# Kernel optimization log

Hardware: AMD Instinct MI355X
Metric: run time of the kernel (lower is better)

Reference implementation:

```python
import jax, jax.numpy as jnp
import numpy as np

B, P, E, H = 16, 1024, 1024, 16
DH = E // H  # 64


def setup_inputs() -> dict:
    key = jax.random.key(0)
    ks = jax.random.split(key, 7)
    # kaiming_uniform on [H, DH, DH]: bound = sqrt(6 / fan_in), fan_in = DH
    bound = float(np.sqrt(6.0 / DH))
    w_att_val = jax.random.uniform(ks[0], (H, DH, DH), jnp.float32, -bound, bound)
    attention_bias = jax.random.normal(ks[1], (H, P, P), jnp.float32)
    lb = float(1.0 / np.sqrt(E))
    wv_w = jax.random.uniform(ks[2], (E, E), jnp.float32, -lb, lb)
    wv_b = jax.random.uniform(ks[3], (E,), jnp.float32, -lb, lb)
    out_w = jax.random.uniform(ks[4], (E, E), jnp.float32, -lb, lb)
    out_b = jax.random.uniform(ks[5], (E,), jnp.float32, -lb, lb)
    x = jax.random.normal(ks[6], (B, P, E), jnp.float32)
    return {"x": x, "w_att_val": w_att_val, "attention_bias": attention_bias,
            "wv_w": wv_w, "wv_b": wv_b, "out_w": out_w, "out_b": out_b}


def reference(x, w_att_val, attention_bias, wv_w, wv_b, out_w, out_b):
    b, p, e = x.shape
    dh = e // H
    # split heads: [B, H, P, DH]
    x_h = x.reshape(b, p, H, dh).transpose(0, 2, 1, 3)
    # bilinear scores: (x_h @ W) @ x_h^T -> [B, H, P, P]
    xw = jnp.einsum('bhpd,hde->bhpe', x_h, w_att_val)
    scores = jnp.einsum('bhpe,bhqe->bhpq', xw, x_h)
    scores = scores / jnp.sqrt(jnp.asarray(dh, x.dtype)) + attention_bias
    attn = jax.nn.softmax(scores, axis=-1)
    # values: Linear(E, E) then split heads
    vx = x @ wv_w.T + wv_b
    vx = vx.reshape(b, p, H, dh).transpose(0, 2, 1, 3)
    out = jnp.einsum('bhpq,bhqd->bhpd', attn, vx)
    out = out.transpose(0, 2, 1, 3).reshape(b, p, e)
    return out @ out_w.T + out_b
```

## Files before the change

### kernel.cpp

```cpp
#include <hip/hip_runtime.h>

#define PB 16
#define PP 1024
#define PE 1024
#define PH 16
#define PDH 64

typedef __attribute__((ext_vector_type(8))) short bf16x8;
typedef __attribute__((ext_vector_type(4))) short bf16x4;
typedef __attribute__((ext_vector_type(4))) float f32x4;

#define LOG2E 1.44269504088896340736f

__device__ __forceinline__ short f2bf(float f) {
    union { float f; unsigned u; } a;
    a.f = f;
    unsigned u = a.u;
    u += 0x7fffu + ((u >> 16) & 1u);
    return (short)(u >> 16);
}
__device__ __forceinline__ float bf2f(short s) {
    union { unsigned u; float f; } a;
    a.u = ((unsigned)(unsigned short)s) << 16;
    return a.f;
}
__device__ __forceinline__ unsigned cvtpk(float lo, float hi) {
    unsigned r;
    asm("v_cvt_pk_bf16_f32 %0, %1, %2" : "=v"(r) : "v"(lo), "v"(hi));
    return r;
}
union U8 { unsigned u[4]; bf16x8 v; };
__device__ __forceinline__ void async16(const void* g, void* l) {
    __builtin_amdgcn_global_load_lds(
        (const __attribute__((address_space(1))) unsigned int*)g,
        (__attribute__((address_space(3))) unsigned int*)l, 16, 0, 0);
}

__global__ __launch_bounds__(256) void bias_conv(const float* __restrict__ bias,
                                                 short* __restrict__ biasb) {
    size_t idx = ((size_t)blockIdx.x * 256 + threadIdx.x) * 8;
    float4 a = *(const float4*)(bias + idx);
    float4 b = *(const float4*)(bias + idx + 4);
    bf16x8 t = {f2bf(a.x * LOG2E), f2bf(a.y * LOG2E), f2bf(a.z * LOG2E), f2bf(a.w * LOG2E),
                f2bf(b.x * LOG2E), f2bf(b.y * LOG2E), f2bf(b.z * LOG2E), f2bf(b.w * LOG2E)};
    *(bf16x8*)(biasb + idx) = t;
}

__global__ __launch_bounds__(256) void wconv(const float* __restrict__ wvw,
                                             const float* __restrict__ outw,
                                             short* __restrict__ wvwb,
                                             short* __restrict__ outwb) {
    int bid = blockIdx.x;
    const float* src = (bid < 512) ? wvw : outw;
    short* dst = (bid < 512) ? wvwb : outwb;
    int lb = (bid < 512) ? bid : bid - 512;
    size_t idx = ((size_t)lb * 256 + threadIdx.x) * 8;
    float4 a = *(const float4*)(src + idx);
    float4 b = *(const float4*)(src + idx + 4);
    bf16x8 t = {f2bf(a.x), f2bf(a.y), f2bf(a.z), f2bf(a.w),
                f2bf(b.x), f2bf(b.y), f2bf(b.z), f2bf(b.w)};
    *(bf16x8*)(dst + idx) = t;
}

__global__ __launch_bounds__(256) void xw_kernel(const float* __restrict__ x,
                                                 const float* __restrict__ watt,
                                                 short* __restrict__ xw,
                                                 short* __restrict__ xbf) {
    int bid = blockIdx.x;
    int q4 = bid & 3;
    int bh = bid >> 2;
    int h = bh & 15;
    __shared__ short Wt[64][88];

    int tid = threadIdx.x;
    {
        const float* W = watt + (size_t)h * 4096;
        int idx = tid * 16;
        int d = idx >> 6, e0 = idx & 63;
#pragma unroll
        for (int i = 0; i < 16; i += 4) {
            float4 v = *(const float4*)(W + d * 64 + e0 + i);
            Wt[e0 + i + 0][d] = f2bf(v.x);
            Wt[e0 + i + 1][d] = f2bf(v.y);
            Wt[e0 + i + 2][d] = f2bf(v.z);
            Wt[e0 + i + 3][d] = f2bf(v.w);
        }
    }
    __syncthreads();

    int wave = tid >> 6, lane = tid & 63;
    int lm = lane & 15, lq = lane >> 4;

    bf16x8 bfr[4][2];
#pragma unroll
    for (int nt = 0; nt < 4; nt++)
#pragma unroll
        for (int kf = 0; kf < 2; kf++)
            bfr[nt][kf] = *(const bf16x8*)&Wt[nt * 16 + lm][kf * 32 + lq * 8];

    int b = bh >> 4;
    const float QSCALE = 0.125f * LOG2E;
    for (int pass = 0; pass < 4; pass++) {
        int p0 = q4 * 256 + pass * 64 + wave * 16;
        const float* xrow = x + ((size_t)(b * 1024 + p0 + lm)) * 1024 + h * 64;
        short* xorow = xbf + ((size_t)(b * 1024 + p0 + lm)) * 1024 + h * 64;
        bf16x8 af[2];
#pragma unroll
        for (int kf = 0; kf < 2; kf++) {
            float4 v0 = *(const float4*)(xrow + kf * 32 + lq * 8);
            float4 v1 = *(const float4*)(xrow + kf * 32 + lq * 8 + 4);
            bf16x8 t;
            t[0] = f2bf(v0.x); t[1] = f2bf(v0.y); t[2] = f2bf(v0.z); t[3] = f2bf(v0.w);
            t[4] = f2bf(v1.x); t[5] = f2bf(v1.y); t[6] = f2bf(v1.z); t[7] = f2bf(v1.w);
            af[kf] = t;
            *(bf16x8*)(xorow + kf * 32 + lq * 8) = t;
        }
#pragma unroll
        for (int nt = 0; nt < 4; nt++) {
            f32x4 acc = {0.f, 0.f, 0.f, 0.f};
            acc = __builtin_amdgcn_mfma_f32_16x16x32_bf16(af[0], bfr[nt][0], acc, 0, 0, 0);
            acc = __builtin_amdgcn_mfma_f32_16x16x32_bf16(af[1], bfr[nt][1], acc, 0, 0, 0);
            size_t base = ((size_t)bh * 1024 + p0 + lq * 4) * 64 + nt * 16 + lm;
#pragma unroll
            for (int r = 0; r < 4; r++)
                xw[base + (size_t)r * 64] = f2bf(acc[r] * QSCALE);
        }
    }
}

__global__ __launch_bounds__(256) void vx_gemm(const short* __restrict__ xbf,
                                               const short* __restrict__ wvwb,
                                               const float* __restrict__ wvb,
                                               short* __restrict__ vt) {
    int mblk = blockIdx.x >> 3, nblk = blockIdx.x & 7;
    int m0 = mblk * 128, n0 = nblk * 128;
    __shared__ short As[128 * 32];
    __shared__ short Bs[128 * 32];

    int tid = threadIdx.x;
    int wv = tid >> 6, ln = tid & 63;
    int c0 = wv * 2;
    int rrow = ln >> 2, rseg = (ln & 3) * 8;
    const short* gA = xbf + (size_t)(m0 + c0 * 16 + rrow) * 1024 + rseg;
    const short* gB = wvwb + (size_t)(n0 + c0 * 16 + rrow) * 1024 + rseg;
    short* lA = As + c0 * 512;
    short* lB = Bs + c0 * 512;

    int lane = ln, lm = lane & 15, lq = lane >> 4;
    int wm = (wv >> 1) * 64, wn = (wv & 1) * 64;

    f32x4 acc[4][4];
#pragma unroll
    for (int i = 0; i < 4; i++)
#pragma unroll
        for (int j = 0; j < 4; j++) acc[i][j] = (f32x4){0.f, 0.f, 0.f, 0.f};

    for (int k0 = 0; k0 < 1024; k0 += 32) {
        __syncthreads();
        async16(gA + k0, lA);
        async16(gA + k0 + 16 * 1024, lA + 512);
        async16(gB + k0, lB);
        async16(gB + k0 + 16 * 1024, lB + 512);
        __syncthreads();
        bf16x8 af[4], bfr[4];
#pragma unroll
        for (int mt = 0; mt < 4; mt++) af[mt] = *(const bf16x8*)&As[(wm + mt * 16 + lm) * 32 + lq * 8];
#pragma unroll
        for (int nt = 0; nt < 4; nt++) bfr[nt] = *(const bf16x8*)&Bs[(wn + nt * 16 + lm) * 32 + lq * 8];
#pragma unroll
        for (int mt = 0; mt < 4; mt++)
#pragma unroll
            for (int nt = 0; nt < 4; nt++)
                acc[mt][nt] = __builtin_amdgcn_mfma_f32_16x16x32_bf16(af[mt], bfr[nt], acc[mt][nt], 0, 0, 0);
    }

#pragma unroll
    for (int nt = 0; nt < 4; nt++) {
        int e = n0 + wn + nt * 16 + lm;
        float bias = wvb[e];
        int hh = e >> 6, dd = e & 63;
#pragma unroll
        for (int mt = 0; mt < 4; mt++) {
            int pg = m0 + wm + mt * 16 + lq * 4;
            int bb = pg >> 10, pp = pg & 1023;
            bf16x4 pk;
#pragma unroll
            for (int r = 0; r < 4; r++) pk[r] = f2bf(acc[mt][nt][r] + bias);
            *(bf16x4*)(vt + ((size_t)((bb * 16 + hh) * 64 + dd)) * 1024 + pp) = pk;
        }
    }
}

__global__ __launch_bounds__(256, 3) void flash_kernel(const short* __restrict__ xbf,
                                                       const short* __restrict__ xw,
                                                       const short* __restrict__ vt,
                                                       const short* __restrict__ biasb,
                                                       short* __restrict__ obuf) {
    int bid = blockIdx.x;
    int qblk = bid & 7, b = (bid >> 3) & 15, h = bid >> 7;
    int bh = b * 16 + h;
    int q0 = qblk * 128;

    __shared__ short Ks[64][72];
    __shared__ short Vs[64][72];
    __shared__ float Rs[4][36];

    int tid = threadIdx.x, wave = tid >> 6, lane = tid & 63;
    int lm = lane & 15, lq = lane >> 4;

    bf16x8 qa[2][2];
#pragma unroll
    for (int qt = 0; qt < 2; qt++)
#pragma unroll
        for (int kf = 0; kf < 2; kf++)
            qa[qt][kf] = *(const bf16x8*)(xw + ((size_t)bh * 1024 + q0 + wave * 32 + qt * 16 + lm) * 64 + kf * 32 + lq * 8);

    f32x4 o[2][4];
#pragma unroll
    for (int qt = 0; qt < 2; qt++)
#pragma unroll
        for (int dt = 0; dt < 4; dt++) o[qt][dt] = (f32x4){0.f, 0.f, 0.f, 0.f};
    float rs[2] = {0.f, 0.f};

    int ci0 = tid * 2, ci1 = tid * 2 + 1;
    int r0 = ci0 >> 3, s0 = (ci0 & 7) * 8;
    int r1 = ci1 >> 3, s1 = (ci1 & 7) * 8;
    const short* kg = xbf + ((size_t)(b * 1024)) * 1024 + h * 64;
    const short* vg = vt + ((size_t)bh * 64) * 1024;
    const short* bg = biasb + ((size_t)h << 20) + (size_t)(q0 + wave * 32) * 1024;

    bf16x8 kr[2], vr[2];
    bf16x4 br[4][2];
    kr[0] = *(const bf16x8*)(kg + (size_t)r0 * 1024 + s0);
    kr[1] = *(const bf16x8*)(kg + (size_t)r1 * 1024 + s1);
    vr[0] = *(const bf16x8*)(vg + (size_t)r0 * 1024 + s0);
    vr[1] = *(const bf16x8*)(vg + (size_t)r1 * 1024 + s1);
#pragma unroll
    for (int kt = 0; kt < 4; kt++)
#pragma unroll
        for (int qt = 0; qt < 2; qt++)
            br[kt][qt] = *(const bf16x4*)(bg + (size_t)(qt * 16 + lm) * 1024 + kt * 16 + lq * 4);
    *(bf16x8*)&Ks[r0][s0] = kr[0];
    *(bf16x8*)&Ks[r1][s1] = kr[1];
    *(bf16x8*)&Vs[r0][s0] = vr[0];
    *(bf16x8*)&Vs[r1][s1] = vr[1];

    for (int tile = 0; tile < 16; tile++) {
        int kv0 = tile * 64;
        __syncthreads();

        f32x4 s[4][2];
#pragma unroll
        for (int kt = 0; kt < 4; kt++)
#pragma unroll
            for (int qt = 0; qt < 2; qt++) {
                bf16x4 bv = br[kt][qt];
                s[kt][qt] = (f32x4){bf2f(bv[0]), bf2f(bv[1]), bf2f(bv[2]), bf2f(bv[3])};
            }

        if (tile < 15) {
            int kvn = kv0 + 64;
            kr[0] = *(const bf16x8*)(kg + (size_t)(kvn + r0) * 1024 + s0);
            kr[1] = *(const bf16x8*)(kg + (size_t)(kvn + r1) * 1024 + s1);
            vr[0] = *(const bf16x8*)(vg + (size_t)r0 * 1024 + kvn + s0);
            vr[1] = *(const bf16x8*)(vg + (size_t)r1 * 1024 + kvn + s1);
#pragma unroll
            for (int kt = 0; kt < 4; kt++)
#pragma unroll
                for (int qt = 0; qt < 2; qt++)
                    br[kt][qt] = *(const bf16x4*)(bg + (size_t)(qt * 16 + lm) * 1024 + kvn + kt * 16 + lq * 4);
        }

#pragma unroll
        for (int kf = 0; kf < 2; kf++) {
            bf16x8 ka[4];
#pragma unroll
            for (int kt = 0; kt < 4; kt++)
                ka[kt] = *(const bf16x8*)&Ks[kt * 16 + lm][kf * 32 + lq * 8];
#pragma unroll
            for (int kt = 0; kt < 4; kt++)
#pragma unroll
                for (int qt = 0; qt < 2; qt++)
                    s[kt][qt] = __builtin_amdgcn_mfma_f32_16x16x32_bf16(ka[kt], qa[qt][kf], s[kt][qt], 0, 0, 0);
        }

#pragma unroll
        for (int kt = 0; kt < 4; kt++)
#pragma unroll
            for (int qt = 0; qt < 2; qt++)
#pragma unroll
                for (int r = 0; r < 4; r++) {
                    float pv = __builtin_amdgcn_exp2f(s[kt][qt][r]);
                    s[kt][qt][r] = pv;
                    rs[qt] += pv;
                }

#pragma unroll
        for (int kf = 0; kf < 2; kf++) {
            bf16x8 pa[2];
#pragma unroll
            for (int qt = 0; qt < 2; qt++) {
                U8 u;
                u.u[0] = cvtpk(s[kf * 2][qt][0], s[kf * 2][qt][1]);
                u.u[1] = cvtpk(s[kf * 2][qt][2], s[kf * 2][qt][3]);
                u.u[2] = cvtpk(s[kf * 2 + 1][qt][0], s[kf * 2 + 1][qt][1]);
                u.u[3] = cvtpk(s[kf * 2 + 1][qt][2], s[kf * 2 + 1][qt][3]);
                pa[qt] = u.v;
            }
#pragma unroll
            for (int dt = 0; dt < 4; dt++) {
                U8 uv;
                *(bf16x4*)&uv.u[0] = *(const bf16x4*)&Vs[dt * 16 + lm][kf * 32 + lq * 4];
                *(bf16x4*)&uv.u[2] = *(const bf16x4*)&Vs[dt * 16 + lm][kf * 32 + 16 + lq * 4];
#pragma unroll
                for (int qt = 0; qt < 2; qt++)
                    o[qt][dt] = __builtin_amdgcn_mfma_f32_16x16x32_bf16(pa[qt], uv.v, o[qt][dt], 0, 0, 0);
            }
        }

        __syncthreads();
        if (tile < 15) {
            *(bf16x8*)&Ks[r0][s0] = kr[0];
            *(bf16x8*)&Ks[r1][s1] = kr[1];
            *(bf16x8*)&Vs[r0][s0] = vr[0];
            *(bf16x8*)&Vs[r1][s1] = vr[1];
        }
    }

#pragma unroll
    for (int qt = 0; qt < 2; qt++) {
        rs[qt] += __shfl_xor(rs[qt], 16);
        rs[qt] += __shfl_xor(rs[qt], 32);
    }
    if (lq == 0) { Rs[wave][lm] = rs[0]; Rs[wave][16 + lm] = rs[1]; }
    __syncthreads();

#pragma unroll
    for (int qt = 0; qt < 2; qt++) {
        float inv[4];
#pragma unroll
        for (int r = 0; r < 4; r++)
            inv[r] = 1.f / Rs[wave][qt * 16 + lq * 4 + r];
#pragma unroll
        for (int dt = 0; dt < 4; dt++) {
            int e = h * 64 + dt * 16 + lm;
#pragma unroll
            for (int r = 0; r < 4; r++) {
                int p = q0 + wave * 32 + qt * 16 + lq * 4 + r;
                obuf[((size_t)(b * 1024 + p)) * 1024 + e] = f2bf(o[qt][dt][r] * inv[r]);
            }
        }
    }
}

__global__ __launch_bounds__(256) void out_gemm(const short* __restrict__ obuf,
                                                const short* __restrict__ outwb,
                                                const float* __restrict__ outb,
                                                float* __restrict__ out) {
    int mblk = blockIdx.x >> 3, nblk = blockIdx.x & 7;
    int m0 = mblk * 128, n0 = nblk * 128;
    __shared__ short As[128 * 32];
    __shared__ short Bs[128 * 32];

    int tid = threadIdx.x;
    int wv = tid >> 6, ln = tid & 63;
    int c0 = wv * 2;
    int rrow = ln >> 2, rseg = (ln & 3) * 8;
    const short* gA = obuf + (size_t)(m0 + c0 * 16 + rrow) * 1024 + rseg;
    const short* gB = outwb + (size_t)(n0 + c0 * 16 + rrow) * 1024 + rseg;
    short* lA = As + c0 * 512;
    short* lB = Bs + c0 * 512;

    int lm = ln & 15, lq = ln >> 4;
    int wm = (wv >> 1) * 64, wn = (wv & 1) * 64;

    f32x4 acc[4][4];
#pragma unroll
    for (int i = 0; i < 4; i++)
#pragma unroll
        for (int j = 0; j < 4; j++) acc[i][j] = (f32x4){0.f, 0.f, 0.f, 0.f};

    for (int k0 = 0; k0 < 1024; k0 += 32) {
        __syncthreads();
        async16(gA + k0, lA);
        async16(gA + k0 + 16 * 1024, lA + 512);
        async16(gB + k0, lB);
        async16(gB + k0 + 16 * 1024, lB + 512);
        __syncthreads();
        bf16x8 af[4], bfr[4];
#pragma unroll
        for (int mt = 0; mt < 4; mt++) af[mt] = *(const bf16x8*)&As[(wm + mt * 16 + lm) * 32 + lq * 8];
#pragma unroll
        for (int nt = 0; nt < 4; nt++) bfr[nt] = *(const bf16x8*)&Bs[(wn + nt * 16 + lm) * 32 + lq * 8];
#pragma unroll
        for (int mt = 0; mt < 4; mt++)
#pragma unroll
            for (int nt = 0; nt < 4; nt++)
                acc[mt][nt] = __builtin_amdgcn_mfma_f32_16x16x32_bf16(af[mt], bfr[nt], acc[mt][nt], 0, 0, 0);
    }

#pragma unroll
    for (int nt = 0; nt < 4; nt++) {
        int e = n0 + wn + nt * 16 + lm;
        float bias = outb[e];
#pragma unroll
        for (int mt = 0; mt < 4; mt++) {
            int pg = m0 + wm + mt * 16 + lq * 4;
#pragma unroll
            for (int r = 0; r < 4; r++)
                out[(size_t)(pg + r) * 1024 + e] = acc[mt][nt][r] + bias;
        }
    }
}

extern "C" void kernel_launch(void* const* d_in, const int* in_sizes, int n_in,
                              void* d_out, int out_size, void* d_ws, size_t ws_size,
                              hipStream_t stream) {
    const float* x    = (const float*)d_in[0];
    const float* watt = (const float*)d_in[1];
    const float* bias = (const float*)d_in[2];
    const float* wvw  = (const float*)d_in[3];
    const float* wvb  = (const float*)d_in[4];
    const float* outw = (const float*)d_in[5];
    const float* outb = (const float*)d_in[6];
    float* out = (float*)d_out;

    char* ws = (char*)d_ws;
    short* xw     = (short*)ws;
    short* vt     = (short*)(ws + ((size_t)32 << 20));
    short* obuf   = (short*)(ws + ((size_t)64 << 20));
    short* biasb  = (short*)(ws + ((size_t)96 << 20));
    short* xbf    = (short*)(ws + ((size_t)128 << 20));
    short* wvwb   = (short*)(ws + ((size_t)160 << 20));
    short* outwb  = (short*)(ws + ((size_t)162 << 20));

    xw_kernel<<<PB * PH * 4, 256, 0, stream>>>(x, watt, xw, xbf);
    bias_conv<<<8192, 256, 0, stream>>>(bias, biasb);
    wconv<<<1024, 256, 0, stream>>>(wvw, outw, wvwb, outwb);
    vx_gemm<<<(PB * PP / 128) * (PE / 128), 256, 0, stream>>>(xbf, wvwb, wvb, vt);
    flash_kernel<<<PB * PH * (PP / 128), 256, 0, stream>>>(xbf, xw, vt, biasb, obuf);
    out_gemm<<<(PB * PP / 128) * (PE / 128), 256, 0, stream>>>(obuf, outwb, outb, out);
}
```

Baseline: 449.8 us.

## Double-buffer K/V tiles with async global-to-LDS copies and an XOR-swizzled layout

Replaces the register-staged single K/V shared tile with two LDS buffers. The next tile is loaded straight into LDS with async16 copies while the current tile is computed, which removes the second barrier and the register round-trip. The padded row layout becomes a 64-wide layout with an XOR swizzle to avoid bank conflicts. The change also wraps the MFMA sections in s_setprio and raises launch bounds to 4 blocks per CU, which tightens the register budget and raises the risk of spills.

Result: slower. 485.2 us (+7.9%).

```diff
diff --git a/kernel.cpp b/kernel.cpp
--- a/kernel.cpp
+++ b/kernel.cpp
@@ -191,7 +191,7 @@
     }
 }
 
-__global__ __launch_bounds__(256, 3) void flash_kernel(const short* __restrict__ xbf,
+__global__ __launch_bounds__(256, 4) void flash_kernel(const short* __restrict__ xbf,
                                                        const short* __restrict__ xw,
                                                        const short* __restrict__ vt,
                                                        const short* __restrict__ biasb,
@@ -201,8 +201,8 @@
     int bh = b * 16 + h;
     int q0 = qblk * 128;
 
-    __shared__ short Ks[64][72];
-    __shared__ short Vs[64][72];
+    __shared__ short Kb[2][64 * 64];
+    __shared__ short Vb[2][64 * 64];
     __shared__ float Rs[4][36];
 
     int tid = threadIdx.x, wave = tid >> 6, lane = tid & 63;
@@ -222,32 +222,44 @@
         for (int dt = 0; dt < 4; dt++) o[qt][dt] = (f32x4){0.f, 0.f, 0.f, 0.f};
     float rs[2] = {0.f, 0.f};
 
-    int ci0 = tid * 2, ci1 = tid * 2 + 1;
-    int r0 = ci0 >> 3, s0 = (ci0 & 7) * 8;
-    int r1 = ci1 >> 3, s1 = (ci1 & 7) * 8;
+    int srow = lane >> 3;
+    int sslot = (lane & 7) ^ srow;
     const short* kg = xbf + ((size_t)(b * 1024)) * 1024 + h * 64;
     const short* vg = vt + ((size_t)bh * 64) * 1024;
+    const short* kp = kg + (size_t)(wave * 16 + srow) * 1024 + sslot * 8;
+    const short* vp = vg + (size_t)(wave * 16 + srow) * 1024 + sslot * 8;
     const short* bg = biasb + ((size_t)h << 20) + (size_t)(q0 + wave * 32) * 1024;
 
-    bf16x8 kr[2], vr[2];
     bf16x4 br[4][2];
-    kr[0] = *(const bf16x8*)(kg + (size_t)r0 * 1024 + s0);
-    kr[1] = *(const bf16x8*)(kg + (size_t)r1 * 1024 + s1);
-    vr[0] = *(const bf16x8*)(vg + (size_t)r0 * 1024 + s0);
-    vr[1] = *(const bf16x8*)(vg + (size_t)r1 * 1024 + s1);
-#pragma unroll
-    for (int kt = 0; kt < 4; kt++)
-#pragma unroll
-        for (int qt = 0; qt < 2; qt++)
-            br[kt][qt] = *(const bf16x4*)(bg + (size_t)(qt * 16 + lm) * 1024 + kt * 16 + lq * 4);
-    *(bf16x8*)&Ks[r0][s0] = kr[0];
-    *(bf16x8*)&Ks[r1][s1] = kr[1];
-    *(bf16x8*)&Vs[r0][s0] = vr[0];
-    *(bf16x8*)&Vs[r1][s1] = vr[1];
+    {
+        short* Kd = Kb[0] + wave * 1024;
+        short* Vd = Vb[0] + wave * 1024;
+        async16(kp, Kd);
+        async16(kp + 8 * 1024, Kd + 512);
+        async16(vp, Vd);
+        async16(vp + 8 * 1024, Vd + 512);
+#pragma unroll
+        for (int kt = 0; kt < 4; kt++)
+#pragma unroll
+            for (int qt = 0; qt < 2; qt++)
+                br[kt][qt] = *(const bf16x4*)(bg + (size_t)(qt * 16 + lm) * 1024 + kt * 16 + lq * 4);
+    }
 
     for (int tile = 0; tile < 16; tile++) {
-        int kv0 = tile * 64;
+        const int cur = tile & 1;
         __syncthreads();
+
+        if (tile < 15) {
+            int kvn = (tile + 1) * 64;
+            short* Kd = Kb[cur ^ 1] + wave * 1024;
+            short* Vd = Vb[cur ^ 1] + wave * 1024;
+            const short* kpn = kp + (size_t)kvn * 1024;
+            const short* vpn = vp + kvn;
+            async16(kpn, Kd);
+            async16(kpn + 8 * 1024, Kd + 512);
+            async16(vpn, Vd);
+            async16(vpn + 8 * 1024, Vd + 512);
+        }
 
         f32x4 s[4][2];
 #pragma unroll
@@ -259,11 +271,7 @@
             }
 
         if (tile < 15) {
-            int kvn = kv0 + 64;
-            kr[0] = *(const bf16x8*)(kg + (size_t)(kvn + r0) * 1024 + s0);
-            kr[1] = *(const bf16x8*)(kg + (size_t)(kvn + r1) * 1024 + s1);
-            vr[0] = *(const bf16x8*)(vg + (size_t)r0 * 1024 + kvn + s0);
-            vr[1] = *(const bf16x8*)(vg + (size_t)r1 * 1024 + kvn + s1);
+            int kvn = (tile + 1) * 64;
 #pragma unroll
             for (int kt = 0; kt < 4; kt++)
 #pragma unroll
@@ -271,18 +279,25 @@
                     br[kt][qt] = *(const bf16x4*)(bg + (size_t)(qt * 16 + lm) * 1024 + kvn + kt * 16 + lq * 4);
         }
 
+        const short* Kc = Kb[cur];
+        const short* Vc = Vb[cur];
+
+        __builtin_amdgcn_s_setprio(1);
 #pragma unroll
         for (int kf = 0; kf < 2; kf++) {
             bf16x8 ka[4];
 #pragma unroll
-            for (int kt = 0; kt < 4; kt++)
-                ka[kt] = *(const bf16x8*)&Ks[kt * 16 + lm][kf * 32 + lq * 8];
+            for (int kt = 0; kt < 4; kt++) {
+                int R = kt * 16 + lm;
+                ka[kt] = *(const bf16x8*)&Kc[R * 64 + (((kf * 4 + lq) ^ (lm & 7)) << 3)];
+            }
 #pragma unroll
             for (int kt = 0; kt < 4; kt++)
 #pragma unroll
                 for (int qt = 0; qt < 2; qt++)
                     s[kt][qt] = __builtin_amdgcn_mfma_f32_16x16x32_bf16(ka[kt], qa[qt][kf], s[kt][qt], 0, 0, 0);
         }
+        __builtin_amdgcn_s_setprio(0);
 
 #pragma unroll
         for (int kt = 0; kt < 4; kt++)
@@ -295,6 +310,7 @@
                     rs[qt] += pv;
                 }
 
+        __builtin_amdgcn_s_setprio(1);
 #pragma unroll
         for (int kf = 0; kf < 2; kf++) {
             bf16x8 pa[2];
@@ -309,22 +325,18 @@
             }
 #pragma unroll
             for (int dt = 0; dt < 4; dt++) {
+                int R = dt * 16 + lm;
                 U8 uv;
-                *(bf16x4*)&uv.u[0] = *(const bf16x4*)&Vs[dt * 16 + lm][kf * 32 + lq * 4];
-                *(bf16x4*)&uv.u[2] = *(const bf16x4*)&Vs[dt * 16 + lm][kf * 32 + 16 + lq * 4];
+                *(bf16x4*)&uv.u[0] = *(const bf16x4*)&Vc[R * 64 +
+                    ((((kf * 4 + (lq >> 1)) ^ (lm & 7)) << 3) + ((lq & 1) << 2))];
+                *(bf16x4*)&uv.u[2] = *(const bf16x4*)&Vc[R * 64 +
+                    ((((kf * 4 + 2 + (lq >> 1)) ^ (lm & 7)) << 3) + ((lq & 1) << 2))];
 #pragma unroll
                 for (int qt = 0; qt < 2; qt++)
                     o[qt][dt] = __builtin_amdgcn_mfma_f32_16x16x32_bf16(pa[qt], uv.v, o[qt][dt], 0, 0, 0);
             }
         }
-
-        __syncthreads();
-        if (tile < 15) {
-            *(bf16x8*)&Ks[r0][s0] = kr[0];
-            *(bf16x8*)&Ks[r1][s1] = kr[1];
-            *(bf16x8*)&Vs[r0][s0] = vr[0];
-            *(bf16x8*)&Vs[r1][s1] = vr[1];
-        }
+        __builtin_amdgcn_s_setprio(0);
     }
 
 #pragma unroll
```
